# Optimization experiments

Hardware: AMD Instinct MI355X
Metric: run time of the kernel (lower is better)

## Reference

```python
import jax, jax.numpy as jnp
import numpy as np
from jax import lax

EPS = 1e-4
DN = ('NDHWC', 'DHWIO', 'NDHWC')


def _m(mask, dtype):
    return mask[..., None].astype(dtype)


def bn_relu(x, mask):
    # BatchNorm1d over active voxels only (training-mode batch stats, gamma=1, beta=0), then ReLU.
    m = _m(mask, x.dtype)
    n = jnp.sum(m)
    mean = jnp.sum(x * m, axis=(0, 1, 2, 3)) / n
    xc = (x - mean) * m  # re-mask: inactive voxels stay exactly zero
    var = jnp.sum(xc * xc, axis=(0, 1, 2, 3)) / n
    return jnp.maximum(xc * lax.rsqrt(var + EPS), 0.0)


def subm3(x, w, mask):
    # SubMConv3d k=3 pad=1: dense conv on zero-at-inactive input, output restricted to active sites.
    y = lax.conv_general_dilated(x, w, (1, 1, 1), 'SAME', dimension_numbers=DN)
    return y * _m(mask, x.dtype)


def down2(x, w):
    # SparseConv3d k=2 s=2: non-overlapping windows; inactive inputs are zero so dense strided conv matches.
    return lax.conv_general_dilated(x, w, (2, 2, 2), 'VALID', dimension_numbers=DN)


def pool_mask(mask):
    B, D, H, W = mask.shape
    return jnp.any(mask.reshape(B, D // 2, 2, H // 2, 2, W // 2, 2), axis=(2, 4, 6))


def up2(x, w, mask):
    # SparseInverseConv3d k=2 (indice_key inverse of the stride-2 conv): conv-transpose masked to original indices.
    y = jnp.einsum('bdhwc,ijkco->bdihjwko', x, w)
    B, Dc, _, Hc, _, Wc, _, Co = y.shape
    return y.reshape(B, 2 * Dc, 2 * Hc, 2 * Wc, Co) * _m(mask, x.dtype)


def resblock(x, mask, wa, wb, w_sc=None):
    # ResidualBlock: i_branch (identity or 1x1 Custom1x1Subm3d: feats @ W.T) + BN-ReLU-SubM-BN-ReLU-SubM.
    idb = x if w_sc is None else jnp.einsum('bdhwc,oc->bdhwo', x, w_sc)
    h = bn_relu(x, mask)
    h = subm3(h, wa, mask)
    h = bn_relu(h, mask)
    h = subm3(h, wb, mask)
    return h + idb


def unet_forward(x, mask, w_in, w_b1a, w_b1b, w_d1, w_b2a, w_b2b, w_d2,
                 w_b3a, w_b3b, w_u2, w_t2_sc, w_t2a, w_t2b, w_u1, w_t1_sc, w_t1a, w_t1b):
    mask2 = pool_mask(mask)
    mask3 = pool_mask(mask2)
    x0 = subm3(x, w_in, mask)                 # input_conv (subm1)
    x1 = resblock(x0, mask, w_b1a, w_b1b)     # level-1 block (32->32)
    d1 = down2(bn_relu(x1, mask), w_d1)       # BN-ReLU + stride-2 conv 32->64
    x2 = resblock(d1, mask2, w_b2a, w_b2b)    # level-2 block (64->64)
    d2 = down2(bn_relu(x2, mask2), w_d2)      # 64->96
    x3 = resblock(d2, mask3, w_b3a, w_b3b)    # bottom level (96->96)
    u2 = up2(bn_relu(x3, mask3), w_u2, mask2)  # BN-ReLU + inverse conv 96->64
    t2 = resblock(jnp.concatenate([x2, u2], -1), mask2, w_t2a, w_t2b, w_t2_sc)  # tail 128->64
    u1 = up2(bn_relu(t2, mask2), w_u1, mask)   # 64->32
    t1 = resblock(jnp.concatenate([x1, u1], -1), mask, w_t1a, w_t1b, w_t1_sc)   # tail 64->32
    return bn_relu(t1, mask)                   # output_layer: BN + ReLU


def setup_inputs() -> dict:
    key = jax.random.key(0)
    ks = jax.random.split(key, 20)
    B, D = 1, 48
    Cin, C1, C2, C3 = 6, 32, 64, 96
    mask = jax.random.uniform(ks[0], (B, D, D, D)) < 0.12
    x = jax.random.normal(ks[1], (B, D, D, D, Cin), jnp.float32) * mask[..., None]

    def w(k, shape):
        fan = float(np.prod(shape[:-1]))
        return (jax.random.normal(k, shape, jnp.float32) / np.sqrt(fan)).astype(jnp.float32)

    return {
        'x': x, 'mask': mask,
        'w_in': w(ks[2], (3, 3, 3, Cin, C1)),
        'w_b1a': w(ks[3], (3, 3, 3, C1, C1)), 'w_b1b': w(ks[4], (3, 3, 3, C1, C1)),
        'w_d1': w(ks[5], (2, 2, 2, C1, C2)),
        'w_b2a': w(ks[6], (3, 3, 3, C2, C2)), 'w_b2b': w(ks[7], (3, 3, 3, C2, C2)),
        'w_d2': w(ks[8], (2, 2, 2, C2, C3)),
        'w_b3a': w(ks[9], (3, 3, 3, C3, C3)), 'w_b3b': w(ks[10], (3, 3, 3, C3, C3)),
        'w_u2': w(ks[11], (2, 2, 2, C3, C2)),
        'w_t2_sc': w(ks[12], (C2, 2 * C2)),
        'w_t2a': w(ks[13], (3, 3, 3, 2 * C2, C2)), 'w_t2b': w(ks[14], (3, 3, 3, C2, C2)),
        'w_u1': w(ks[15], (2, 2, 2, C2, C1)),
        'w_t1_sc': w(ks[16], (C1, 2 * C1)),
        'w_t1a': w(ks[17], (3, 3, 3, 2 * C1, C1)), 'w_t1b': w(ks[18], (3, 3, 3, C1, C1)),
    }


def reference(x, mask, w_in, w_b1a, w_b1b, w_d1, w_b2a, w_b2b, w_d2,
              w_b3a, w_b3b, w_u2, w_t2_sc, w_t2a, w_t2b, w_u1, w_t1_sc, w_t1a, w_t1b):
    return unet_forward(x, mask, w_in, w_b1a, w_b1b, w_d1, w_b2a, w_b2b, w_d2,
                        w_b3a, w_b3b, w_u2, w_t2_sc, w_t2a, w_t2b, w_u1, w_t1_sc, w_t1a, w_t1b)
```

## Files before the change

### kernel.cpp

```cpp
#include <hip/hip_runtime.h>


typedef short bf16x8 __attribute__((ext_vector_type(8)));
typedef float f32x4 __attribute__((ext_vector_type(4)));
typedef unsigned short ushort_t;

constexpr int D1 = 48, DIM2 = 24, DIM3 = 12;
constexpr int N1 = D1 * D1 * D1;
constexpr int N2 = DIM2 * DIM2 * DIM2;
constexpr int N3 = DIM3 * DIM3 * DIM3;

constexpr size_t OFF_A      = 0;
constexpr size_t OFF_R1     = 3538944;
constexpr size_t OFF_CAT1   = 7077888;
constexpr size_t OFF_D1R    = 14155776;
constexpr size_t OFF_R3     = 15040512;
constexpr size_t OFF_CAT2   = 15925248;
constexpr size_t OFF_D2R    = 17694720;
constexpr size_t OFF_R4     = 17860608;
constexpr size_t OFF_X3R    = 18026496;
constexpr size_t OFF_BN1_32 = 18192384;
constexpr size_t OFF_BN1_64 = 19961920;
constexpr size_t OFF_BN2_A  = 23500928;
constexpr size_t OFF_BN2_B  = 23943360;
constexpr size_t OFF_BN3_96 = 24385792;
constexpr size_t OFF_BFEND  = 24468800;
constexpr size_t OFF_WT     = 24468800;
constexpr size_t OFF_STATS  = 25142592;
constexpr size_t STATS_FLOATS = 16 * 4096;
constexpr size_t OFF_CNT    = OFF_STATS + STATS_FLOATS;
constexpr size_t OFF_L1     = OFF_CNT + 16;
constexpr size_t OFF_L2     = OFF_L1 + N1;
constexpr size_t OFF_L3     = OFF_L2 + N2;
constexpr size_t OFF_M1     = OFF_L3 + N3;
constexpr size_t OFF_M2     = OFF_M1 + N1 / 4;
constexpr size_t OFF_M3     = OFF_M2 + N2 / 4;

constexpr int WTS[17] = {0, 27648, 55296, 82944, 99328, 209920, 320512,
                         369664, 618496, 867328, 977920, 1088512, 1199104,
                         1254400, 1282048, 1331200, 1347584};

__device__ inline ushort_t f2bf(float f) {
  union { float f; unsigned u; } x; x.f = f;
  unsigned u = x.u + 0x7FFF + ((x.u >> 16) & 1);
  return (ushort_t)(u >> 16);
}

__global__ __launch_bounds__(256) void k_mask1(const float* __restrict__ x,
                                               unsigned char* __restrict__ m,
                                               int* __restrict__ list, int* __restrict__ cnt) {
  int v = blockIdx.x * 256 + threadIdx.x;
  if (v >= N1) return;
  const float* p = x + (size_t)v * 6;
  bool a = (p[0] != 0.f) || (p[1] != 0.f) || (p[2] != 0.f) ||
           (p[3] != 0.f) || (p[4] != 0.f) || (p[5] != 0.f);
  m[v] = a ? 1 : 0;
  if (a) { int pos = atomicAdd(cnt, 1); list[pos] = v; }
}

__global__ __launch_bounds__(256) void k_pool(const unsigned char* __restrict__ mf,
                                              unsigned char* __restrict__ mc,
                                              int* __restrict__ list, int* __restrict__ cnt, int DC) {
  int v = blockIdx.x * 256 + threadIdx.x;
  int n = DC * DC * DC;
  if (v >= n) return;
  int w = v % DC, h = (v / DC) % DC, d = v / (DC * DC);
  int DF = 2 * DC;
  bool a = false;
  for (int i = 0; i < 2; i++)
    for (int j = 0; j < 2; j++)
      for (int k = 0; k < 2; k++)
        a |= (mf[(size_t)(((2 * d + i) * DF + (2 * h + j)) * DF + (2 * w + k))] != 0);
  mc[v] = a ? 1 : 0;
  if (a) { int pos = atomicAdd(cnt, 1); list[pos] = v; }
}

struct WJobs {
  const float* src[16];
  int start[17];
  short cirtot[16], cio[16], cipad[16], cout[16];
};

__global__ __launch_bounds__(256) void k_wprep(WJobs jb, ushort_t* __restrict__ wt, int total) {
  int gid = blockIdx.x * 256 + threadIdx.x;
  if (gid >= total) return;
  int j = 0;
#pragma unroll
  for (int jj = 0; jj < 16; jj++)
    if (gid >= jb.start[jj + 1]) j = jj + 1;
  int e = gid - jb.start[j];
  int CIP = jb.cipad[j], CO = jb.cout[j];
  int CIRT = jb.cirtot[j], CIO = jb.cio[j];
  int ci = e % CIP;
  int co = (e / CIP) % CO;
  int k = e / (CIP * CO);
  float v = (ci + CIO < CIRT) ? jb.src[j][((size_t)k * CIRT + CIO + ci) * CO + co] : 0.f;
  wt[gid] = f2bf(v);
}

__global__ __launch_bounds__(256) void k_xprep(const float* __restrict__ x, ushort_t* __restrict__ xp) {
  int gid = blockIdx.x * 256 + threadIdx.x;
  if (gid >= (N1 + 4) * 8) return;
  int v = gid >> 3, c = (gid & 7) * 4;
  uint2 o = make_uint2(0u, 0u);
  if (v < N1) {
    ushort_t u[4];
#pragma unroll
    for (int j = 0; j < 4; j++) {
      int ci = c + j;
      float f = (ci < 6) ? x[(size_t)v * 6 + ci] : 0.f;
      u[j] = f2bf(f);
    }
    o.x = (unsigned)u[0] | ((unsigned)u[1] << 16);
    o.y = (unsigned)u[2] | ((unsigned)u[3] << 16);
  }
  *(uint2*)&xp[(size_t)v * 32 + c] = o;
}

template <int CIPAD, int CB, int KK, int VG, int DD, bool UP>
__global__ __launch_bounds__(512, 2) void k_conv8(
    const ushort_t* __restrict__ in, const ushort_t* __restrict__ wt, int cot,
    float* __restrict__ out, int ostride, int ooff,
    const float* __restrict__ res, int rstride,
    double* __restrict__ st,
    const int* __restrict__ list, const int* __restrict__ cnt) {
  constexpr int KCH = CIPAD / 32;
  constexpr int NCO = CB / 16;
  constexpr int KS = 8 / VG;
  constexpr int TPS = (KK + KS - 1) / KS;
  constexpr int TILE = VG * 16;
  constexpr int ETOT = VG * NCO * 256;
  constexpr int NE = (ETOT + 511) / 512;
  __shared__ float red[KS][VG][NCO * 4][64];
  __shared__ float sred0[CB], sred1[CB];
  __shared__ int vidx[TILE];

  int n = cnt[0];
  int t = threadIdx.x, wv = t >> 6, ln = t & 63;
  int vg = wv % VG, ks = wv / VG;
  int fr = ln & 15, kg = ln >> 4;
  int coblk = blockIdx.y * CB;
  int k0 = ks * TPS;

  bf16x8 wr[TPS][KCH][NCO];
#pragma unroll
  for (int j = 0; j < TPS; j++) {
    int kk = k0 + j;
    int kc = (kk < KK) ? kk : KK - 1;
#pragma unroll
    for (int c = 0; c < KCH; c++)
#pragma unroll
      for (int f = 0; f < NCO; f++)
        wr[j][c][f] = *(const bf16x8*)(wt +
            ((size_t)kc * cot + coblk + f * 16 + fr) * CIPAD + c * 32 + kg * 8);
  }
  if (t < CB) { sred0[t] = 0.f; sred1[t] = 0.f; }

  float smr = 0.f, sqr = 0.f;
  int myco = ((t >> 8) % NCO) * 16 + (t & 15);

  constexpr int GDI = UP ? (DD / 2) : ((KK == 8) ? 2 * DD : DD);
  constexpr int SENT = GDI * GDI * GDI;

  for (int tile = blockIdx.x; tile * TILE < n; tile += gridDim.x) {
    int base = tile * TILE;
    if (t < TILE) vidx[t] = (base + t < n) ? list[base + t] : -1;
    __syncthreads();

    int av = vidx[vg * 16 + fr];
    int vv = av < 0 ? 0 : av;
    int ad = vv / (DD * DD), ah = (vv / DD) % DD, aw = vv % DD;
    int pidx = 0, corner = -1;
    if (UP) {
      constexpr int DC = DD / 2;
      pidx = (((ad >> 1) * DC) + (ah >> 1)) * DC + (aw >> 1);
      corner = ((ad & 1) << 2) | ((ah & 1) << 1) | (aw & 1);
    }

    auto nixOf = [&](int kq) -> int {
      int kc = (kq < KK) ? kq : KK - 1;
      bool tapv = (kq < KK) && (av >= 0);
      if (UP) {
        return (tapv && corner == kc) ? pidx : SENT;
      } else if (KK == 27) {
        int kd = kc / 9 - 1, kh = (kc / 3) % 3 - 1, kw = kc % 3 - 1;
        int nd = ad + kd, nh = ah + kh, nw = aw + kw;
        bool inb = tapv && (unsigned)nd < (unsigned)DD &&
                   (unsigned)nh < (unsigned)DD && (unsigned)nw < (unsigned)DD;
        return inb ? (nd * DD + nh) * DD + nw : SENT;
      } else {
        return tapv ? ((2 * ad + ((kc >> 2) & 1)) * GDI + (2 * ah + ((kc >> 1) & 1))) * GDI +
                          (2 * aw + (kc & 1))
                    : SENT;
      }
    };
    auto loadA = [&](bf16x8* dst, int j) {
      int nix = nixOf(k0 + j);
      const ushort_t* ap = in + (size_t)nix * CIPAD + kg * 8;
#pragma unroll
      for (int c = 0; c < KCH; c++) dst[c] = *(const bf16x8*)(ap + c * 32);
    };

    f32x4 acc[NCO];
#pragma unroll
    for (int f = 0; f < NCO; f++) acc[f] = (f32x4){0.f, 0.f, 0.f, 0.f};

    bf16x8 aA[KCH], aB[KCH];
    loadA(aA, 0);
#pragma unroll
    for (int j = 0; j < TPS; j++) {
      if (j + 1 < TPS) loadA((j & 1) ? aA : aB, j + 1);
      bf16x8* cur = (j & 1) ? aB : aA;
#pragma unroll
      for (int c = 0; c < KCH; c++)
#pragma unroll
        for (int f = 0; f < NCO; f++)
          acc[f] = __builtin_amdgcn_mfma_f32_16x16x32_bf16(cur[c], wr[j][c][f], acc[f], 0, 0, 0);
    }

#pragma unroll
    for (int f = 0; f < NCO; f++)
#pragma unroll
      for (int r = 0; r < 4; r++)
        red[ks][vg][f * 4 + r][ln] = acc[f][r];
    __syncthreads();

#pragma unroll
    for (int e0 = 0; e0 < NE; e0++) {
      int e = t + e0 * 512;
      if (e < ETOT) {
        int ln2 = e & 63, r = (e >> 6) & 3;
        int f = (e >> 8) % NCO;
        int vg2 = e / (256 * NCO);
        float s = 0.f;
#pragma unroll
        for (int q = 0; q < KS; q++) s += red[q][vg2][f * 4 + r][ln2];
        int slot = vg2 * 16 + (ln2 >> 4) * 4 + r;
        int co = f * 16 + (ln2 & 15);
        int v = vidx[slot];
        if (v >= 0) {
          int gco = coblk + co;
          float val = s;
          if (res) val += res[(size_t)v * rstride + gco];
          out[(size_t)v * ostride + ooff + gco] = val;
          smr += val; sqr += val * val;
        }
      }
    }
    __syncthreads();
  }

  atomicAdd(&sred0[myco], smr);
  atomicAdd(&sred1[myco], sqr);
  __syncthreads();
  if (t < CB) {
    double* sr = st + (size_t)(blockIdx.x & 7) * 256;
    atomicAdd(&sr[coblk + t], (double)sred0[t]);
    atomicAdd(&sr[128 + coblk + t], (double)sred1[t]);
  }
}

template <int C>
__global__ __launch_bounds__(256) void k_bnapply2(
    const float* __restrict__ x, int xstr, int coff,
    const double* __restrict__ sA, const double* __restrict__ sB, int csplit,
    const int* __restrict__ list, const int* __restrict__ cnt,
    ushort_t* __restrict__ out) {
  __shared__ float mu_s[C], inv_s[C];
  int n = cnt[0];
  int t = threadIdx.x;
  if (t < C) {
    const double* s = (t < csplit) ? (sA + t) : (sB + (t - csplit));
    double sm = 0.0, sq = 0.0;
#pragma unroll
    for (int r = 0; r < 8; r++) { sm += s[r * 256]; sq += s[r * 256 + 128]; }
    double mu = sm / n;
    double var = sq / n - mu * mu;
    mu_s[t] = (float)mu;
    inv_s[t] = rsqrtf((float)fmax(var, 0.0) + 1e-4f);
  }
  __syncthreads();
  int total = n * (C / 4);
  for (int gid = blockIdx.x * 256 + t; gid < total; gid += gridDim.x * 256) {
    int i = gid / (C / 4);
    int c = (gid % (C / 4)) * 4;
    int v = list[i];
    float4 xv = *(const float4*)&x[(size_t)v * xstr + coff + c];
    float xa[4] = {xv.x, xv.y, xv.z, xv.w};
    ushort_t u[4];
#pragma unroll
    for (int j = 0; j < 4; j++)
      u[j] = f2bf(fmaxf((xa[j] - mu_s[c + j]) * inv_s[c + j], 0.f));
    uint2 o; o.x = (unsigned)u[0] | ((unsigned)u[1] << 16);
    o.y = (unsigned)u[2] | ((unsigned)u[3] << 16);
    *(uint2*)&out[(size_t)v * C + c] = o;
  }
}

__global__ __launch_bounds__(256) void k_bnout(const float* __restrict__ x,
                                               const unsigned char* __restrict__ m,
                                               const double* __restrict__ s,
                                               const int* __restrict__ cnt,
                                               float* __restrict__ out) {
  __shared__ float mu_s[32], inv_s[32];
  int t = threadIdx.x;
  int n = cnt[0];
  if (t < 32) {
    double sm = 0.0, sq = 0.0;
#pragma unroll
    for (int r = 0; r < 8; r++) { sm += s[r * 256 + t]; sq += s[r * 256 + 128 + t]; }
    double mu = sm / n;
    double var = sq / n - mu * mu;
    mu_s[t] = (float)mu;
    inv_s[t] = rsqrtf((float)fmax(var, 0.0) + 1e-4f);
  }
  __syncthreads();
  int gid = blockIdx.x * 256 + t;
  if (gid >= N1 * 8) return;
  int v = gid / 8;
  int c = (gid % 8) * 4;
  float4 o = make_float4(0.f, 0.f, 0.f, 0.f);
  if (m[v]) {
    float4 xv = *(const float4*)&x[(size_t)v * 32 + c];
    o.x = fmaxf((xv.x - mu_s[c + 0]) * inv_s[c + 0], 0.f);
    o.y = fmaxf((xv.y - mu_s[c + 1]) * inv_s[c + 1], 0.f);
    o.z = fmaxf((xv.z - mu_s[c + 2]) * inv_s[c + 2], 0.f);
    o.w = fmaxf((xv.w - mu_s[c + 3]) * inv_s[c + 3], 0.f);
  }
  *(float4*)&out[(size_t)v * 32 + c] = o;
}

template <int CI, int CO>
__global__ __launch_bounds__(256) void k_sc(const float* __restrict__ in,
                                            const float* __restrict__ wsc,
                                            float* __restrict__ out,
                                            const int* __restrict__ list,
                                            const int* __restrict__ cnt) {
  int n = cnt[0];
  long total = (long)n * CO;
  for (long gid = (long)blockIdx.x * 256 + threadIdx.x; gid < total; gid += (long)gridDim.x * 256) {
    int i = (int)(gid / CO), o = (int)(gid % CO);
    int v = list[i];
    const float4* xr = (const float4*)(in + (size_t)v * CI);
    const float4* wr = (const float4*)(wsc + (size_t)o * CI);
    float a = 0.f;
    for (int c = 0; c < CI / 4; c++) {
      float4 x4 = xr[c], w4 = wr[c];
      a += x4.x * w4.x + x4.y * w4.y + x4.z * w4.z + x4.w * w4.w;
    }
    out[(size_t)v * CO + o] = a;
  }
}

extern "C" void kernel_launch(void* const* d_in, const int* in_sizes, int n_in,
                              void* d_out, int out_size, void* d_ws, size_t ws_size,
                              hipStream_t stream) {
  float* W = (float*)d_ws;
  const float* x = (const float*)d_in[0];

  float* A    = W + OFF_A;
  float* R1   = W + OFF_R1;
  float* CAT1 = W + OFF_CAT1;
  float* D1R  = W + OFF_D1R;
  float* R3   = W + OFF_R3;
  float* CAT2 = W + OFF_CAT2;
  float* D2R  = W + OFF_D2R;
  float* R4   = W + OFF_R4;
  float* X3R  = W + OFF_X3R;
  ushort_t* XP     = (ushort_t*)(W + OFF_CAT1);
  ushort_t* BN1_32 = (ushort_t*)(W + OFF_BN1_32);
  ushort_t* BN1_64 = (ushort_t*)(W + OFF_BN1_64);
  ushort_t* BN2A   = (ushort_t*)(W + OFF_BN2_A);
  ushort_t* BN2B   = (ushort_t*)(W + OFF_BN2_B);
  ushort_t* BN3_96 = (ushort_t*)(W + OFF_BN3_96);
  ushort_t* WT  = (ushort_t*)(W + OFF_WT);
  double* S0 = (double*)(W + OFF_STATS);
  int* CNT = (int*)(W + OFF_CNT);
  int* L1 = (int*)(W + OFF_L1);
  int* L2 = (int*)(W + OFF_L2);
  int* L3 = (int*)(W + OFF_L3);
  unsigned char* M1 = (unsigned char*)(W + OFF_M1);
  unsigned char* M2 = (unsigned char*)(W + OFF_M2);
  unsigned char* M3 = (unsigned char*)(W + OFF_M3);

  auto S = [&](int i) { return S0 + (size_t)i * 2048; };

  hipMemsetAsync(W + OFF_STATS, 0, (STATS_FLOATS + 16) * 4, stream);
  hipMemsetAsync(W + OFF_BN1_32, 0, (OFF_BFEND - OFF_BN1_32) * 4, stream);

  k_mask1<<<N1 / 256, 256, 0, stream>>>(x, M1, L1, CNT + 0);
  k_pool<<<N2 / 256, 256, 0, stream>>>(M1, M2, L2, CNT + 1, DIM2);
  k_pool<<<(N3 + 255) / 256, 256, 0, stream>>>(M2, M3, L3, CNT + 2, DIM3);

  WJobs jb;
  const int srcIdx[16]  = {2, 3, 4, 5, 6, 7, 8, 9, 10, 13, 13, 14, 17, 18, 11, 15};
  const short cirtot[16]= {6, 32, 32, 32, 64, 64, 64, 96, 96, 128, 128, 64, 64, 32, 96, 64};
  const short cio[16]   = {0, 0, 0, 0, 0, 0, 0, 0, 0, 0, 64, 0, 0, 0, 0, 0};
  const short cipad[16] = {32, 32, 32, 32, 64, 64, 64, 96, 96, 64, 64, 64, 64, 32, 96, 64};
  const short couts[16] = {32, 32, 32, 64, 64, 64, 96, 96, 96, 64, 64, 64, 32, 32, 64, 32};
  for (int j = 0; j < 16; j++) {
    jb.src[j] = (const float*)d_in[srcIdx[j]];
    jb.cirtot[j] = cirtot[j]; jb.cio[j] = cio[j];
    jb.cipad[j] = cipad[j]; jb.cout[j] = couts[j];
    jb.start[j] = WTS[j];
  }
  jb.start[16] = WTS[16];
  k_wprep<<<(WTS[16] + 255) / 256, 256, 0, stream>>>(jb, WT, WTS[16]);
  k_xprep<<<((N1 + 4) * 8 + 255) / 256, 256, 0, stream>>>(x, XP);

  const int BNG = 512;

  k_conv8<32, 32, 27, 2, D1, false><<<dim3(256, 1), 512, 0, stream>>>(
      XP, WT + WTS[0], 32, A, 32, 0, nullptr, 0, S(0), L1, CNT + 0);
  k_bnapply2<32><<<BNG, 256, 0, stream>>>(A, 32, 0, S(0), S(0), 32, L1, CNT + 0, BN1_32);
  k_conv8<32, 32, 27, 2, D1, false><<<dim3(256, 1), 512, 0, stream>>>(
      BN1_32, WT + WTS[1], 32, R1, 32, 0, nullptr, 0, S(1), L1, CNT + 0);
  k_bnapply2<32><<<BNG, 256, 0, stream>>>(R1, 32, 0, S(1), S(1), 32, L1, CNT + 0, BN1_32);
  k_conv8<32, 32, 27, 2, D1, false><<<dim3(256, 1), 512, 0, stream>>>(
      BN1_32, WT + WTS[2], 32, CAT1, 64, 0, A, 32, S(2), L1, CNT + 0);
  k_bnapply2<32><<<BNG, 256, 0, stream>>>(CAT1, 64, 0, S(2), S(2), 32, L1, CNT + 0, BN1_32);
  k_conv8<32, 32, 8, 2, DIM2, false><<<dim3(160, 2), 512, 0, stream>>>(
      BN1_32, WT + WTS[3], 64, D1R, 64, 0, nullptr, 0, S(3), L2, CNT + 1);

  k_bnapply2<64><<<BNG, 256, 0, stream>>>(D1R, 64, 0, S(3), S(3), 64, L2, CNT + 1, BN2A);
  k_conv8<64, 16, 27, 2, DIM2, false><<<dim3(96, 4), 512, 0, stream>>>(
      BN2A, WT + WTS[4], 64, R3, 64, 0, nullptr, 0, S(4), L2, CNT + 1);
  k_bnapply2<64><<<BNG, 256, 0, stream>>>(R3, 64, 0, S(4), S(4), 64, L2, CNT + 1, BN2A);
  k_conv8<64, 16, 27, 2, DIM2, false><<<dim3(96, 4), 512, 0, stream>>>(
      BN2A, WT + WTS[5], 64, CAT2, 128, 0, D1R, 64, S(5), L2, CNT + 1);
  k_bnapply2<64><<<BNG, 256, 0, stream>>>(CAT2, 128, 0, S(5), S(5), 64, L2, CNT + 1, BN2A);
  k_conv8<64, 32, 8, 2, DIM3, false><<<dim3(54, 3), 512, 0, stream>>>(
      BN2A, WT + WTS[6], 96, D2R, 96, 0, nullptr, 0, S(6), L3, CNT + 2);

  k_bnapply2<96><<<BNG, 256, 0, stream>>>(D2R, 96, 0, S(6), S(6), 96, L3, CNT + 2, BN3_96);
  k_conv8<96, 16, 27, 1, DIM3, false><<<dim3(108, 6), 512, 0, stream>>>(
      BN3_96, WT + WTS[7], 96, R4, 96, 0, nullptr, 0, S(7), L3, CNT + 2);
  k_bnapply2<96><<<BNG, 256, 0, stream>>>(R4, 96, 0, S(7), S(7), 96, L3, CNT + 2, BN3_96);
  k_conv8<96, 16, 27, 1, DIM3, false><<<dim3(108, 6), 512, 0, stream>>>(
      BN3_96, WT + WTS[8], 96, X3R, 96, 0, D2R, 96, S(8), L3, CNT + 2);
  k_bnapply2<96><<<BNG, 256, 0, stream>>>(X3R, 96, 0, S(8), S(8), 96, L3, CNT + 2, BN3_96);
  k_conv8<96, 32, 8, 2, DIM2, true><<<dim3(160, 2), 512, 0, stream>>>(
      BN3_96, WT + WTS[14], 64, CAT2, 128, 64, nullptr, 0, S(9), L2, CNT + 1);

  k_bnapply2<64><<<BNG, 256, 0, stream>>>(CAT2, 128, 64, S(9), S(9), 64, L2, CNT + 1, BN2B);
  k_conv8<64, 16, 27, 2, DIM2, false><<<dim3(96, 4), 512, 0, stream>>>(
      BN2A, WT + WTS[9], 64, R3, 64, 0, nullptr, 0, S(15), L2, CNT + 1);
  k_conv8<64, 16, 27, 2, DIM2, false><<<dim3(96, 4), 512, 0, stream>>>(
      BN2B, WT + WTS[10], 64, R3, 64, 0, R3, 64, S(10), L2, CNT + 1);
  k_bnapply2<64><<<BNG, 256, 0, stream>>>(R3, 64, 0, S(10), S(10), 64, L2, CNT + 1, BN2A);
  k_sc<128, 64><<<512, 256, 0, stream>>>(CAT2, (const float*)d_in[12], D1R, L2, CNT + 1);
  k_conv8<64, 16, 27, 2, DIM2, false><<<dim3(96, 4), 512, 0, stream>>>(
      BN2A, WT + WTS[11], 64, R3, 64, 0, D1R, 64, S(11), L2, CNT + 1);
  k_bnapply2<64><<<BNG, 256, 0, stream>>>(R3, 64, 0, S(11), S(11), 64, L2, CNT + 1, BN2A);
  k_conv8<64, 32, 8, 2, D1, true><<<dim3(256, 1), 512, 0, stream>>>(
      BN2A, WT + WTS[15], 32, CAT1, 64, 32, nullptr, 0, S(12), L1, CNT + 0);

  k_bnapply2<64><<<BNG, 256, 0, stream>>>(CAT1, 64, 0, S(2), S(12), 32, L1, CNT + 0, BN1_64);
  k_conv8<64, 16, 27, 2, D1, false><<<dim3(256, 2), 512, 0, stream>>>(
      BN1_64, WT + WTS[12], 32, R1, 32, 0, nullptr, 0, S(13), L1, CNT + 0);
  k_bnapply2<32><<<BNG, 256, 0, stream>>>(R1, 32, 0, S(13), S(13), 32, L1, CNT + 0, BN1_32);
  k_sc<64, 32><<<512, 256, 0, stream>>>(CAT1, (const float*)d_in[16], A, L1, CNT + 0);
  k_conv8<32, 32, 27, 2, D1, false><<<dim3(256, 1), 512, 0, stream>>>(
      BN1_32, WT + WTS[13], 32, A, 32, 0, A, 32, S(14), L1, CNT + 0);
  k_bnout<<<N1 * 8 / 256, 256, 0, stream>>>(A, M1, S(14), CNT + 0, (float*)d_out);
}
```

Measured before the change: 423.6 us.

## Split conv taps across all 8 waves with 16-voxel tiles and wider channel blocks

Restructures the gathered MFMA sparse conv so every block handles 16 active voxels and all 8 waves divide the kernel taps in a strided pattern (ks + 8j), removing the VG voxel-group dimension. Channel blocks for the 64-channel convs grow from 16 to 32, the grids get larger, and an empty asm barrier keeps the weight fragments in registers. The aim is better tap-level load balance, fewer redundant activation gathers per output channel, and more blocks for latency hiding. In exchange each tile now needs an 8-way cross-wave reduction through LDS, and the larger per-thread register footprint could limit occupancy.

```diff
diff --git a/kernel.cpp b/kernel.cpp
--- a/kernel.cpp
+++ b/kernel.cpp
@@ -46,6 +46,8 @@
   return (ushort_t)(u >> 16);
 }
 
+#define KEEP8(x) asm volatile("" : "+v"(x))
+
 __global__ __launch_bounds__(256) void k_mask1(const float* __restrict__ x,
                                                unsigned char* __restrict__ m,
                                                int* __restrict__ list, int* __restrict__ cnt) {
@@ -117,8 +119,8 @@
   *(uint2*)&xp[(size_t)v * 32 + c] = o;
 }
 
-template <int CIPAD, int CB, int KK, int VG, int DD, bool UP>
-__global__ __launch_bounds__(512, 2) void k_conv8(
+template <int CIPAD, int CB, int KK, int DD, bool UP>
+__global__ __launch_bounds__(512, 2) void k_conv12(
     const ushort_t* __restrict__ in, const ushort_t* __restrict__ wt, int cot,
     float* __restrict__ out, int ostride, int ooff,
     const float* __restrict__ res, int rstride,
@@ -126,26 +128,21 @@
     const int* __restrict__ list, const int* __restrict__ cnt) {
   constexpr int KCH = CIPAD / 32;
   constexpr int NCO = CB / 16;
-  constexpr int KS = 8 / VG;
-  constexpr int TPS = (KK + KS - 1) / KS;
-  constexpr int TILE = VG * 16;
-  constexpr int ETOT = VG * NCO * 256;
-  constexpr int NE = (ETOT + 511) / 512;
-  __shared__ float red[KS][VG][NCO * 4][64];
-  __shared__ float sred0[CB], sred1[CB];
-  __shared__ int vidx[TILE];
-
-  int n = cnt[0];
-  int t = threadIdx.x, wv = t >> 6, ln = t & 63;
-  int vg = wv % VG, ks = wv / VG;
-  int fr = ln & 15, kg = ln >> 4;
-  int coblk = blockIdx.y * CB;
-  int k0 = ks * TPS;
+  constexpr int TPS = (KK + 7) / 8;
+  constexpr int ETOT = NCO * 256;
+  __shared__ float red[8][NCO * 4][64];
+  __shared__ float sred[2 * CB];
+  __shared__ int vidx[16];
+
+  const int n = cnt[0];
+  const int t = threadIdx.x, ks = t >> 6, ln = t & 63;
+  const int fr = ln & 15, kg = ln >> 4;
+  const int coblk = blockIdx.y * CB;
 
   bf16x8 wr[TPS][KCH][NCO];
 #pragma unroll
   for (int j = 0; j < TPS; j++) {
-    int kk = k0 + j;
+    int kk = ks + j * 8;
     int kc = (kk < KK) ? kk : KK - 1;
 #pragma unroll
     for (int c = 0; c < KCH; c++)
@@ -154,20 +151,25 @@
         wr[j][c][f] = *(const bf16x8*)(wt +
             ((size_t)kc * cot + coblk + f * 16 + fr) * CIPAD + c * 32 + kg * 8);
   }
-  if (t < CB) { sred0[t] = 0.f; sred1[t] = 0.f; }
+#pragma unroll
+  for (int j = 0; j < TPS; j++)
+#pragma unroll
+    for (int c = 0; c < KCH; c++)
+#pragma unroll
+      for (int f = 0; f < NCO; f++) KEEP8(wr[j][c][f]);
+
+  if (t < 2 * CB) sred[t] = 0.f;
 
   float smr = 0.f, sqr = 0.f;
-  int myco = ((t >> 8) % NCO) * 16 + (t & 15);
-
   constexpr int GDI = UP ? (DD / 2) : ((KK == 8) ? 2 * DD : DD);
   constexpr int SENT = GDI * GDI * GDI;
 
-  for (int tile = blockIdx.x; tile * TILE < n; tile += gridDim.x) {
-    int base = tile * TILE;
-    if (t < TILE) vidx[t] = (base + t < n) ? list[base + t] : -1;
+  for (int tile = blockIdx.x; tile * 16 < n; tile += gridDim.x) {
+    int base = tile * 16;
+    if (t < 16) vidx[t] = (base + t < n) ? list[base + t] : -1;
     __syncthreads();
 
-    int av = vidx[vg * 16 + fr];
+    int av = vidx[fr];
     int vv = av < 0 ? 0 : av;
     int ad = vv / (DD * DD), ah = (vv / DD) % DD, aw = vv % DD;
     int pidx = 0, corner = -1;
@@ -195,7 +197,7 @@
       }
     };
     auto loadA = [&](bf16x8* dst, int j) {
-      int nix = nixOf(k0 + j);
+      int nix = nixOf(ks + j * 8);
       const ushort_t* ap = in + (size_t)nix * CIPAD + kg * 8;
 #pragma unroll
       for (int c = 0; c < KCH; c++) dst[c] = *(const bf16x8*)(ap + c * 32);
@@ -222,41 +224,40 @@
     for (int f = 0; f < NCO; f++)
 #pragma unroll
       for (int r = 0; r < 4; r++)
-        red[ks][vg][f * 4 + r][ln] = acc[f][r];
+        red[ks][f * 4 + r][ln] = acc[f][r];
     __syncthreads();
 
-#pragma unroll
-    for (int e0 = 0; e0 < NE; e0++) {
-      int e = t + e0 * 512;
-      if (e < ETOT) {
-        int ln2 = e & 63, r = (e >> 6) & 3;
-        int f = (e >> 8) % NCO;
-        int vg2 = e / (256 * NCO);
-        float s = 0.f;
-#pragma unroll
-        for (int q = 0; q < KS; q++) s += red[q][vg2][f * 4 + r][ln2];
-        int slot = vg2 * 16 + (ln2 >> 4) * 4 + r;
-        int co = f * 16 + (ln2 & 15);
-        int v = vidx[slot];
-        if (v >= 0) {
-          int gco = coblk + co;
-          float val = s;
-          if (res) val += res[(size_t)v * rstride + gco];
-          out[(size_t)v * ostride + ooff + gco] = val;
-          smr += val; sqr += val * val;
-        }
+    if (t < ETOT) {
+      int ln2 = t & 63, r = (t >> 6) & 3;
+      int f = (t >> 8);
+      float sv = 0.f;
+#pragma unroll
+      for (int q = 0; q < 8; q++) sv += red[q][f * 4 + r][ln2];
+      int slot = (ln2 >> 4) * 4 + r;
+      int ii = base + slot;
+      int v = (ii < n) ? list[ii] : -1;
+      if (v >= 0) {
+        int gco = coblk + f * 16 + (ln2 & 15);
+        float val = sv;
+        if (res) val += res[(size_t)v * rstride + gco];
+        out[(size_t)v * ostride + ooff + gco] = val;
+        smr += val;
+        sqr += val * val;
       }
     }
     __syncthreads();
   }
 
-  atomicAdd(&sred0[myco], smr);
-  atomicAdd(&sred1[myco], sqr);
+  if (t < ETOT) {
+    int myco = (t >> 8) * 16 + (t & 15);
+    atomicAdd(&sred[myco], smr);
+    atomicAdd(&sred[CB + myco], sqr);
+  }
   __syncthreads();
   if (t < CB) {
-    double* sr = st + (size_t)(blockIdx.x & 7) * 256;
-    atomicAdd(&sr[coblk + t], (double)sred0[t]);
-    atomicAdd(&sr[128 + coblk + t], (double)sred1[t]);
+    double* sr = st + (size_t)((int)blockIdx.x & 7) * 256;
+    atomicAdd(&sr[coblk + t], (double)sred[t]);
+    atomicAdd(&sr[128 + coblk + t], (double)sred[CB + t]);
   }
 }
 
@@ -410,57 +411,57 @@
 
   const int BNG = 512;
 
-  k_conv8<32, 32, 27, 2, D1, false><<<dim3(256, 1), 512, 0, stream>>>(
+  k_conv12<32, 32, 27, D1, false><<<dim3(448, 1), 512, 0, stream>>>(
       XP, WT + WTS[0], 32, A, 32, 0, nullptr, 0, S(0), L1, CNT + 0);
   k_bnapply2<32><<<BNG, 256, 0, stream>>>(A, 32, 0, S(0), S(0), 32, L1, CNT + 0, BN1_32);
-  k_conv8<32, 32, 27, 2, D1, false><<<dim3(256, 1), 512, 0, stream>>>(
+  k_conv12<32, 32, 27, D1, false><<<dim3(448, 1), 512, 0, stream>>>(
       BN1_32, WT + WTS[1], 32, R1, 32, 0, nullptr, 0, S(1), L1, CNT + 0);
   k_bnapply2<32><<<BNG, 256, 0, stream>>>(R1, 32, 0, S(1), S(1), 32, L1, CNT + 0, BN1_32);
-  k_conv8<32, 32, 27, 2, D1, false><<<dim3(256, 1), 512, 0, stream>>>(
+  k_conv12<32, 32, 27, D1, false><<<dim3(448, 1), 512, 0, stream>>>(
       BN1_32, WT + WTS[2], 32, CAT1, 64, 0, A, 32, S(2), L1, CNT + 0);
   k_bnapply2<32><<<BNG, 256, 0, stream>>>(CAT1, 64, 0, S(2), S(2), 32, L1, CNT + 0, BN1_32);
-  k_conv8<32, 32, 8, 2, DIM2, false><<<dim3(160, 2), 512, 0, stream>>>(
+  k_conv12<32, 32, 8, DIM2, false><<<dim3(320, 2), 512, 0, stream>>>(
       BN1_32, WT + WTS[3], 64, D1R, 64, 0, nullptr, 0, S(3), L2, CNT + 1);
 
   k_bnapply2<64><<<BNG, 256, 0, stream>>>(D1R, 64, 0, S(3), S(3), 64, L2, CNT + 1, BN2A);
-  k_conv8<64, 16, 27, 2, DIM2, false><<<dim3(96, 4), 512, 0, stream>>>(
+  k_conv12<64, 32, 27, DIM2, false><<<dim3(320, 2), 512, 0, stream>>>(
       BN2A, WT + WTS[4], 64, R3, 64, 0, nullptr, 0, S(4), L2, CNT + 1);
   k_bnapply2<64><<<BNG, 256, 0, stream>>>(R3, 64, 0, S(4), S(4), 64, L2, CNT + 1, BN2A);
-  k_conv8<64, 16, 27, 2, DIM2, false><<<dim3(96, 4), 512, 0, stream>>>(
+  k_conv12<64, 32, 27, DIM2, false><<<dim3(320, 2), 512, 0, stream>>>(
       BN2A, WT + WTS[5], 64, CAT2, 128, 0, D1R, 64, S(5), L2, CNT + 1);
   k_bnapply2<64><<<BNG, 256, 0, stream>>>(CAT2, 128, 0, S(5), S(5), 64, L2, CNT + 1, BN2A);
-  k_conv8<64, 32, 8, 2, DIM3, false><<<dim3(54, 3), 512, 0, stream>>>(
+  k_conv12<64, 32, 8, DIM3, false><<<dim3(108, 3), 512, 0, stream>>>(
       BN2A, WT + WTS[6], 96, D2R, 96, 0, nullptr, 0, S(6), L3, CNT + 2);
 
   k_bnapply2<96><<<BNG, 256, 0, stream>>>(D2R, 96, 0, S(6), S(6), 96, L3, CNT + 2, BN3_96);
-  k_conv8<96, 16, 27, 1, DIM3, false><<<dim3(108, 6), 512, 0, stream>>>(
+  k_conv12<96, 16, 27, DIM3, false><<<dim3(108, 6), 512, 0, stream>>>(
       BN3_96, WT + WTS[7], 96, R4, 96, 0, nullptr, 0, S(7), L3, CNT + 2);
   k_bnapply2<96><<<BNG, 256, 0, stream>>>(R4, 96, 0, S(7), S(7), 96, L3, CNT + 2, BN3_96);
-  k_conv8<96, 16, 27, 1, DIM3, false><<<dim3(108, 6), 512, 0, stream>>>(
+  k_conv12<96, 16, 27, DIM3, false><<<dim3(108, 6), 512, 0, stream>>>(
       BN3_96, WT + WTS[8], 96, X3R, 96, 0, D2R, 96, S(8), L3, CNT + 2);
   k_bnapply2<96><<<BNG, 256, 0, stream>>>(X3R, 96, 0, S(8), S(8), 96, L3, CNT + 2, BN3_96);
-  k_conv8<96, 32, 8, 2, DIM2, true><<<dim3(160, 2), 512, 0, stream>>>(
+  k_conv12<96, 32, 8, DIM2, true><<<dim3(320, 2), 512, 0, stream>>>(
       BN3_96, WT + WTS[14], 64, CAT2, 128, 64, nullptr, 0, S(9), L2, CNT + 1);
 
   k_bnapply2<64><<<BNG, 256, 0, stream>>>(CAT2, 128, 64, S(9), S(9), 64, L2, CNT + 1, BN2B);
-  k_conv8<64, 16, 27, 2, DIM2, false><<<dim3(96, 4), 512, 0, stream>>>(
+  k_conv12<64, 32, 27, DIM2, false><<<dim3(320, 2), 512, 0, stream>>>(
       BN2A, WT + WTS[9], 64, R3, 64, 0, nullptr, 0, S(15), L2, CNT + 1);
-  k_conv8<64, 16, 27, 2, DIM2, false><<<dim3(96, 4), 512, 0, stream>>>(
+  k_conv12<64, 32, 27, DIM2, false><<<dim3(320, 2), 512, 0, stream>>>(
       BN2B, WT + WTS[10], 64, R3, 64, 0, R3, 64, S(10), L2, CNT + 1);
   k_bnapply2<64><<<BNG, 256, 0, stream>>>(R3, 64, 0, S(10), S(10), 64, L2, CNT + 1, BN2A);
   k_sc<128, 64><<<512, 256, 0, stream>>>(CAT2, (const float*)d_in[12], D1R, L2, CNT + 1);
-  k_conv8<64, 16, 27, 2, DIM2, false><<<dim3(96, 4), 512, 0, stream>>>(
+  k_conv12<64, 32, 27, DIM2, false><<<dim3(320, 2), 512, 0, stream>>>(
       BN2A, WT + WTS[11], 64, R3, 64, 0, D1R, 64, S(11), L2, CNT + 1);
   k_bnapply2<64><<<BNG, 256, 0, stream>>>(R3, 64, 0, S(11), S(11), 64, L2, CNT + 1, BN2A);
-  k_conv8<64, 32, 8, 2, D1, true><<<dim3(256, 1), 512, 0, stream>>>(
+  k_conv12<64, 32, 8, D1, true><<<dim3(448, 1), 512, 0, stream>>>(
       BN2A, WT + WTS[15], 32, CAT1, 64, 32, nullptr, 0, S(12), L1, CNT + 0);
 
   k_bnapply2<64><<<BNG, 256, 0, stream>>>(CAT1, 64, 0, S(2), S(12), 32, L1, CNT + 0, BN1_64);
-  k_conv8<64, 16, 27, 2, D1, false><<<dim3(256, 2), 512, 0, stream>>>(
+  k_conv12<64, 32, 27, D1, false><<<dim3(448, 1), 512, 0, stream>>>(
       BN1_64, WT + WTS[12], 32, R1, 32, 0, nullptr, 0, S(13), L1, CNT + 0);
   k_bnapply2<32><<<BNG, 256, 0, stream>>>(R1, 32, 0, S(13), S(13), 32, L1, CNT + 0, BN1_32);
   k_sc<64, 32><<<512, 256, 0, stream>>>(CAT1, (const float*)d_in[16], A, L1, CNT + 0);
-  k_conv8<32, 32, 27, 2, D1, false><<<dim3(256, 1), 512, 0, stream>>>(
+  k_conv12<32, 32, 27, D1, false><<<dim3(448, 1), 512, 0, stream>>>(
       BN1_32, WT + WTS[13], 32, A, 32, 0, A, 32, S(14), L1, CNT + 0);
   k_bnout<<<N1 * 8 / 256, 256, 0, stream>>>(A, M1, S(14), CNT + 0, (float*)d_out);
 }
```

Result: faster. 413.6 us (-2.3%).
